# Performance work log

Hardware: AMD Instinct MI355X
Metric: run time of the kernel (lower is better)

## Reference

```python
import jax, jax.numpy as jnp
import numpy as np

PI = 3.141592653589793
DET_THRESHOLD = 0.25
MAX_DET = 100
REG_HEAD = 4
DEPTH_MEAN = 28.01  # smoke_coder.depth_ref[0]
DIM_REF = (3.88, 1.63, 1.53)  # smoke_coder.dim_ref[0] (l, h, w)


def setup_inputs() -> dict:
    key = jax.random.key(0)
    k1, k2, k3, k4 = jax.random.split(key, 4)
    B, C, H, W = 32, 3, 256, 832  # stride-4 feature map of 3328x1024 images
    pred_heatmap = jax.random.uniform(k1, (B, C, H, W), dtype=jnp.float32)
    pred_regression = jax.random.normal(k2, (B, C + 1, H, W), dtype=jnp.float32) * 0.1  # REG_HEAD=4 channels
    trans_mat = jnp.tile(jnp.array([[0.25, 0.0, 0.0], [0.0, 0.25, 0.0], [0.0, 0.0, 1.0]], jnp.float32), (B, 1, 1))
    K_mat = jnp.tile(jnp.array([[2100.0, 0.0, 1664.0], [0.0, 2100.0, 512.0], [0.0, 0.0, 1.0]], jnp.float32), (B, 1, 1))
    size = jnp.tile(jnp.array([3328.0, 1024.0], jnp.float32), (B, 1))  # (img_w, img_h)
    h_cam = jax.random.uniform(k3, (B,), jnp.float32, 1.4, 2.0)
    dimensions = jax.random.uniform(k4, (B, 3), jnp.float32, 1.5, 4.0)
    return dict(pred_heatmap=pred_heatmap, pred_regression=pred_regression, trans_mat=trans_mat,
                K_mat=K_mat, size=size, h_cam=h_cam, dimensions=dimensions)


def reference(pred_heatmap, pred_regression, trans_mat, K_mat, size, h_cam, dimensions):
    B, C, H, W = pred_heatmap.shape
    K = MAX_DET
    # ---- nms_hm: 3x3 max-pool, keep local maxima ----
    hmax = jax.lax.reduce_window(pred_heatmap, -jnp.inf, jax.lax.max, (1, 1, 3, 3), (1, 1, 1, 1), 'SAME')
    heat = pred_heatmap * (hmax == pred_heatmap).astype(pred_heatmap.dtype)
    # ---- select_topk: per-class topk then global topk ----
    scores_c, inds_c = jax.lax.top_k(heat.reshape(B, C, H * W), K)  # [B,C,K]
    ys_c = (inds_c // W).astype(jnp.float32)
    xs_c = (inds_c % W).astype(jnp.float32)
    scores, topk_ind = jax.lax.top_k(scores_c.reshape(B, C * K), K)  # [B,K]
    clses = (topk_ind // K).astype(jnp.float32)
    inds = jnp.take_along_axis(inds_c.reshape(B, C * K), topk_ind, axis=1)
    ys = jnp.take_along_axis(ys_c.reshape(B, C * K), topk_ind, axis=1)
    xs = jnp.take_along_axis(xs_c.reshape(B, C * K), topk_ind, axis=1)
    feat = pred_regression.reshape(B, REG_HEAD, H * W).transpose(0, 2, 1)  # [B,HW,R]
    pois = jnp.take_along_axis(feat, inds[:, :, None], axis=1).reshape(-1, REG_HEAD)  # [B*K,R]
    log_dv_delta = pois[:, 0]
    off_u = pois[:, 1]
    ori = pois[:, 2:]
    # ---- feature points -> image points via inverse affine ----
    pts = jnp.stack([xs.reshape(-1), ys.reshape(-1)], axis=1)
    pts = pts + jnp.stack([off_u, jnp.zeros_like(off_u)], axis=1)
    pts_h = jnp.concatenate([pts, jnp.ones((pts.shape[0], 1), pts.dtype)], axis=1)  # [N,3]
    obj = jnp.repeat(jnp.arange(B), K)
    trans_inv = jnp.linalg.inv(trans_mat)[obj]  # [N,3,3]
    img_pts = jnp.einsum('nij,nj->ni', trans_inv, pts_h)[:, :2]
    # ---- per-object camera params ----
    Ks = K_mat[obj]
    h = h_cam[obj]
    kd = dimensions[obj]
    fx, fy, cx = Ks[:, 0, 0], Ks[:, 1, 1], Ks[:, 0, 2]
    dim_ref = jnp.array(DIM_REF, jnp.float32)
    dims = jnp.where(jnp.isfinite(kd), kd, dim_ref[None, :])
    # ---- geometric depth decode ----
    h_ref = h - dims[:, 1] / 2.0
    log_dv_ref = jnp.log(jnp.clip(fy * jnp.abs(h_ref), 1e-7, None) / DEPTH_MEAN)
    log_dv = jnp.clip(log_dv_ref + log_dv_delta, -4.0, 8.0)
    depths = jnp.clip(fy * jnp.abs(h_ref) * jnp.exp(-log_dv), 0.5, 120.0)
    px = (img_pts[:, 0] - cx) * depths / fx
    locs = jnp.stack([px, h, depths], axis=1)  # [N,3]
    # ---- decode_orientation (SMOKE) ----
    rays = jnp.arctan(locs[:, 0] / (locs[:, 2] + 1e-7))
    alphas = jnp.arctan(ori[:, 0] / (ori[:, 1] + 1e-7))
    alphas = alphas + jnp.where(ori[:, 1] >= 0, -PI / 2, PI / 2)
    rotys = alphas + rays
    rotys = jnp.where(rotys > PI, rotys - 2 * PI, rotys)
    rotys = jnp.where(rotys < -PI, rotys + 2 * PI, rotys)
    # ---- encode_box2d: build 3D corners, rotate, project, clamp ----
    cos, sin = jnp.cos(rotys), jnp.sin(rotys)
    cx8 = jnp.array([-0.5, 0.5, 0.5, 0.5, 0.5, -0.5, -0.5, -0.5], jnp.float32)
    cy8 = jnp.array([-1.0, -1.0, 0.0, 0.0, -1.0, -1.0, 0.0, 0.0], jnp.float32)
    cz8 = jnp.array([-0.5, -0.5, -0.5, 0.5, 0.5, 0.5, 0.5, -0.5], jnp.float32)
    xc = dims[:, 0:1] * cx8  # l
    yc = dims[:, 1:2] * cy8  # h
    zc = dims[:, 2:3] * cz8  # w
    bx = cos[:, None] * xc + sin[:, None] * zc
    bz = -sin[:, None] * xc + cos[:, None] * zc
    box3d = jnp.stack([bx, yc, bz], axis=1) + locs[:, :, None]  # [N,3,8]
    proj = jnp.einsum('nij,njk->nik', Ks, box3d)
    uv = proj[:, :2, :] / proj[:, 2:3, :]
    img_w = size.reshape(-1)[0]
    img_h = size.reshape(-1)[1]
    xmins = jnp.clip(jnp.min(uv[:, 0, :], axis=1), 0.0, img_w)
    xmaxs = jnp.clip(jnp.max(uv[:, 0, :], axis=1), 0.0, img_w)
    ymins = jnp.clip(jnp.min(uv[:, 1, :], axis=1), 0.0, img_h)
    ymaxs = jnp.clip(jnp.max(uv[:, 1, :], axis=1), 0.0, img_h)
    box2d = jnp.stack([xmins, ymins, xmaxs, ymaxs], axis=1)
    pred_dims = jnp.roll(dims, -1, axis=1)  # (l,h,w)->(h,w,l)
    result = jnp.concatenate([clses.reshape(-1, 1), alphas[:, None], box2d, pred_dims, locs,
                              rotys[:, None], scores.reshape(-1, 1)], axis=1)  # [N,14]
    # fixed-shape equivalent of boolean filtering: zero out rows below threshold
    keep = (result[:, -1] > DET_THRESHOLD).astype(result.dtype)
    return result * keep[:, None]
```

## Files before the change

kernel.cpp:

```cpp
#include <hip/hip_runtime.h>
#include <math.h>

#define B_ 32
#define C_ 3
#define H_ 256
#define W_ 832
#define HW_ (H_*W_)
#define K_ 100
#define RPB 16
#define PARTS (H_/RPB)
#define NLOAD (W_/4)
#define BLK 256
#define CAP 2048
#define NCAND (C_*PARTS*K_)

typedef unsigned long long ull;

template<int N>
__device__ inline void bitonic_sort_desc(ull* s) {
    for (int k = 2; k <= N; k <<= 1) {
        for (int j = k >> 1; j > 0; j >>= 1) {
            __syncthreads();
            for (int i = threadIdx.x; i < N; i += BLK) {
                int ixj = i ^ j;
                if (ixj > i) {
                    ull a = s[i], b = s[ixj];
                    bool up = ((i & k) == 0);
                    if (up ? (a < b) : (a > b)) { s[i] = b; s[ixj] = a; }
                }
            }
        }
    }
    __syncthreads();
}

__device__ ull radix_select(const ull* __restrict__ buf, int cnt, int k) {
    __shared__ unsigned hist[256];
    __shared__ unsigned wsum[4];
    __shared__ ull pref_s;
    __shared__ int k_s;
    const int tid = threadIdx.x;
    const int lane = tid & 63;
    const int wv = tid >> 6;
    if (cnt < k) return 0ULL;
    if (tid == 0) { pref_s = 0ULL; k_s = k; }

    for (int pos = 7; pos >= 0; --pos) {
        __syncthreads();
        hist[tid] = 0;
        __syncthreads();
        const ull prefix = pref_s;
        const int kk = k_s;
        for (int i0 = 0; i0 < cnt; i0 += BLK) {
            const int i = i0 + tid;
            ull key = (i < cnt) ? buf[i] : 0ULL;
            bool todo = (i < cnt) &&
                        ((pos == 7) || ((key >> (8 * (pos + 1))) == prefix));
            unsigned d = (unsigned)(key >> (8 * pos)) & 255u;
            #pragma unroll
            for (int it = 0; it < 4; ++it) {
                const ull act = __ballot(todo);
                if (act == 0ULL) break;
                const int leader = __ffsll((long long)act) - 1;
                const unsigned dl = (unsigned)__shfl((int)d, leader);
                const bool same = todo && (d == dl);
                const ull ms = __ballot(same);
                if (lane == leader) atomicAdd(&hist[dl], (unsigned)__popcll(ms));
                if (same) todo = false;
            }
            if (todo) atomicAdd(&hist[d], 1u);
        }
        __syncthreads();
        const unsigned h = hist[tid];
        unsigned v = h;
        #pragma unroll
        for (int off = 1; off < 64; off <<= 1) {
            const unsigned o = __shfl_down(v, off);
            if (lane + off < 64) v += o;
        }
        if (lane == 0) wsum[wv] = v;
        __syncthreads();
        unsigned carry = 0;
        #pragma unroll
        for (int w = 0; w < 4; ++w) if (w > wv) carry += wsum[w];
        const unsigned S = v + carry;
        const unsigned above = S - h;
        if (S >= (unsigned)kk && above < (unsigned)kk) {
            pref_s = (prefix << 8) | (ull)tid;
            k_s = kk - (int)above;
        }
    }
    __syncthreads();
    return pref_s;
}

__global__ void __launch_bounds__(BLK) topk_part_kernel(
        const float* __restrict__ heat, ull* __restrict__ part_out) {
    const int chan = blockIdx.x / PARTS;
    const int c    = chan % C_;
    const int part = blockIdx.x % PARTS;
    const float* __restrict__ hp = heat + (size_t)chan * HW_;
    const int r0 = part * RPB;
    const int tid = threadIdx.x;
    const bool active = tid < NLOAD;
    const int x4 = tid * 4;
    const int lane = tid & 63;

    __shared__ float vmA[W_], vmB[W_];
    __shared__ ull buf[CAP];
    __shared__ int cnt;
    if (tid == 0) cnt = 0;

    float4 rA, rB, rC, rD;
    if (active) {
        const int ym1 = (r0 == 0) ? 0 : r0 - 1;
        rA = reinterpret_cast<const float4*>(hp + (size_t)ym1 * W_)[tid];
        rB = reinterpret_cast<const float4*>(hp + (size_t)r0  * W_)[tid];
        const int yp1 = (r0 == H_ - 1) ? r0 : r0 + 1;
        rC = reinterpret_cast<const float4*>(hp + (size_t)yp1 * W_)[tid];
    }
    __syncthreads();

    for (int r = 0; r < RPB; ++r) {
        const int y = r0 + r;
        float* vr = (r & 1) ? vmB : vmA;
        float4 vm;
        if (active) {
            const int yn = (y + 2 > H_ - 1) ? H_ - 1 : y + 2;
            rD = reinterpret_cast<const float4*>(hp + (size_t)yn * W_)[tid];
            vm.x = fmaxf(fmaxf(rA.x, rB.x), rC.x);
            vm.y = fmaxf(fmaxf(rA.y, rB.y), rC.y);
            vm.z = fmaxf(fmaxf(rA.z, rB.z), rC.z);
            vm.w = fmaxf(fmaxf(rA.w, rB.w), rC.w);
            reinterpret_cast<float4*>(&vr[x4])[0] = vm;
        }
        __syncthreads();
        {
            float left = -INFINITY, right = -INFINITY;
            float vv0 = 0.f, vv1 = 0.f, vv2 = 0.f, vv3 = 0.f;
            if (active) {
                left  = (tid == 0)         ? -INFINITY : vr[x4 - 1];
                right = (tid == NLOAD - 1) ? -INFINITY : vr[x4 + 4];
                vv0 = rB.x; vv1 = rB.y; vv2 = rB.z; vv3 = rB.w;
            }
            const float vn[6] = {left, vm.x, vm.y, vm.z, vm.w, right};
            const float vv[4] = {vv0, vv1, vv2, vv3};
            #pragma unroll
            for (int i = 0; i < 4; ++i) {
                const float v = vv[i];
                const bool peak = active && (v >= vn[i]) && (v >= vn[i+1]) && (v >= vn[i+2]);
                const ull m = __ballot(peak);
                if (peak) {
                    const unsigned p = (unsigned)(y * W_ + x4 + i);
                    const unsigned tie = ((unsigned)c << 18) | p;
                    const ull key = ((ull)__float_as_uint(v) << 32) | (ull)(~tie);
                    const int rank = __popcll(m & ((1ULL << lane) - 1ULL));
                    const int leader = __ffsll((long long)m) - 1;
                    int base = 0;
                    if (lane == leader) base = atomicAdd(&cnt, (int)__popcll(m));
                    base = __shfl(base, leader);
                    const int pos = base + rank;
                    if (pos < CAP) buf[pos] = key;
                }
            }
        }
        rA = rB; rB = rC; rC = rD;
    }
    __syncthreads();

    const int cc = (cnt < CAP) ? cnt : CAP;
    const ull thr = radix_select(buf, cc, K_);

    __shared__ int ocnt;
    if (tid == 0) ocnt = 0;
    __syncthreads();
    ull* o = part_out + (size_t)blockIdx.x * K_;
    for (int i0 = 0; i0 < cc; i0 += BLK) {
        const int i = i0 + tid;
        const ull key = (i < cc) ? buf[i] : 0ULL;
        const bool sel = (i < cc) && (key >= thr) && (key != 0ULL);
        const ull m = __ballot(sel);
        const int nsel = (int)__popcll(m);
        int base = 0;
        if (lane == 0 && nsel) base = atomicAdd(&ocnt, nsel);
        base = __shfl(base, 0);
        const int rank = (int)__popcll(m & ((1ULL << lane) - 1ULL));
        if (sel && base + rank < K_) o[base + rank] = key;
    }
    __syncthreads();
    const int oc = (ocnt < K_) ? ocnt : K_;
    for (int i = oc + tid; i < K_; i += BLK) o[i] = 0ULL;
}

__global__ void __launch_bounds__(BLK) merge_geom_kernel(
        const ull* __restrict__ part_keys, const float* __restrict__ reg,
        const float* __restrict__ trans, const float* __restrict__ Km,
        const float* __restrict__ sz, const float* __restrict__ hcam,
        const float* __restrict__ dimen, float* __restrict__ out) {
    const int b = blockIdx.x;
    const int tid = threadIdx.x;
    const int lane = tid & 63;
    __shared__ ull buf[NCAND];
    __shared__ ull sel_s[128];
    __shared__ int ocnt;
    const ull* src = part_keys + (size_t)b * NCAND;
    for (int i = tid; i < NCAND; i += BLK) buf[i] = src[i];
    if (tid < 128) sel_s[tid] = 0ULL;
    if (tid == 0) ocnt = 0;
    __syncthreads();

    const ull thr = radix_select(buf, NCAND, K_);
    for (int i0 = 0; i0 < NCAND; i0 += BLK) {
        const int i = i0 + tid;
        const ull key = (i < NCAND) ? buf[i] : 0ULL;
        const bool sel = (i < NCAND) && (key >= thr) && (key != 0ULL);
        const ull m = __ballot(sel);
        const int nsel = (int)__popcll(m);
        int base = 0;
        if (lane == 0 && nsel) base = atomicAdd(&ocnt, nsel);
        base = __shfl(base, 0);
        const int rank = (int)__popcll(m & ((1ULL << lane) - 1ULL));
        if (sel && base + rank < 128) sel_s[base + rank] = key;
    }
    bitonic_sort_desc<128>(sel_s);

    if (tid >= K_) return;
    const int n = b * K_ + tid;
    const ull key = sel_s[tid];
    const unsigned tie = ~(unsigned)(key & 0xFFFFFFFFULL);
    const float score = __uint_as_float((unsigned)(key >> 32));
    const float clsf  = (float)((tie >> 18) & 3u);
    unsigned hw = tie & 0x3FFFFu;
    if (hw >= HW_) hw = 0;
    const float xs = (float)(hw % W_);
    const float ys = (float)(hw / W_);

    const float* rg = reg + (size_t)b * 4 * HW_;
    const float delta = rg[hw];
    const float off_u = rg[HW_ + hw];
    const float ori0  = rg[2 * HW_ + hw];
    const float ori1  = rg[3 * HW_ + hw];

    const float* T = trans + b * 9;
    const float t00=T[0], t01=T[1], t02=T[2], t10=T[3], t11=T[4], t12=T[5],
                t20=T[6], t21=T[7], t22=T[8];
    const float det3 = t00*(t11*t22 - t12*t21) - t01*(t10*t22 - t12*t20)
                     + t02*(t10*t21 - t11*t20);
    const float idt = 1.0f / det3;
    const float i00 = (t11*t22 - t12*t21)*idt;
    const float i01 = (t02*t21 - t01*t22)*idt;
    const float i02 = (t01*t12 - t02*t11)*idt;

    const float pu = xs + off_u;
    const float img_x = i00*pu + i01*ys + i02;

    const float* Kb = Km + b * 9;
    const float k00=Kb[0],k01=Kb[1],k02=Kb[2],k10=Kb[3],k11=Kb[4],k12=Kb[5],
                k20=Kb[6],k21=Kb[7],k22=Kb[8];
    const float fx = k00, fy = k11, cx = k02;
    const float h = hcam[b];
    float d0 = dimen[b*3+0], d1 = dimen[b*3+1], d2 = dimen[b*3+2];
    if (!isfinite(d0)) d0 = 3.88f;
    if (!isfinite(d1)) d1 = 1.63f;
    if (!isfinite(d2)) d2 = 1.53f;

    const float h_ref = h - d1 * 0.5f;
    const float fyh = fy * fabsf(h_ref);
    const float log_dv_ref = logf(fmaxf(fyh, 1e-7f) / 28.01f);
    const float log_dv = fminf(fmaxf(log_dv_ref + delta, -4.0f), 8.0f);
    const float depth = fminf(fmaxf(fyh * expf(-log_dv), 0.5f), 120.0f);
    const float px = (img_x - cx) * depth / fx;

    const float PI_F = 3.14159265358979323846f;
    const float ray = atanf(px / (depth + 1e-7f));
    float alpha = atanf(ori0 / (ori1 + 1e-7f));
    alpha += (ori1 >= 0.0f) ? -1.5707963267948966f : 1.5707963267948966f;
    float roty = alpha + ray;
    if (roty >  PI_F) roty -= 6.283185307179586f;
    if (roty < -PI_F) roty += 6.283185307179586f;

    const float cosr = cosf(roty), sinr = sinf(roty);
    const float cx8[8] = {-0.5f, 0.5f, 0.5f, 0.5f, 0.5f,-0.5f,-0.5f,-0.5f};
    const float cy8[8] = {-1.0f,-1.0f, 0.0f, 0.0f,-1.0f,-1.0f, 0.0f, 0.0f};
    const float cz8[8] = {-0.5f,-0.5f,-0.5f, 0.5f, 0.5f, 0.5f, 0.5f,-0.5f};
    float umin = 1e30f, umax = -1e30f, vmin = 1e30f, vmax = -1e30f;
    #pragma unroll
    for (int i = 0; i < 8; ++i) {
        const float xc = d0 * cx8[i];
        const float yc = d1 * cy8[i];
        const float zc = d2 * cz8[i];
        const float X = cosr*xc + sinr*zc + px;
        const float Y = yc + h;
        const float Z = -sinr*xc + cosr*zc + depth;
        const float w = k20*X + k21*Y + k22*Z;
        const float u = (k00*X + k01*Y + k02*Z) / w;
        const float v = (k10*X + k11*Y + k12*Z) / w;
        umin = fminf(umin, u); umax = fmaxf(umax, u);
        vmin = fminf(vmin, v); vmax = fmaxf(vmax, v);
    }
    const float img_w = sz[0], img_h = sz[1];
    const float xmin = fminf(fmaxf(umin, 0.0f), img_w);
    const float xmax = fminf(fmaxf(umax, 0.0f), img_w);
    const float ymin = fminf(fmaxf(vmin, 0.0f), img_h);
    const float ymax = fminf(fmaxf(vmax, 0.0f), img_h);

    const float keep = (score > 0.25f) ? 1.0f : 0.0f;
    float* o = out + (size_t)n * 14;
    o[0]  = clsf  * keep;
    o[1]  = alpha * keep;
    o[2]  = xmin  * keep;
    o[3]  = ymin  * keep;
    o[4]  = xmax  * keep;
    o[5]  = ymax  * keep;
    o[6]  = d1    * keep;
    o[7]  = d2    * keep;
    o[8]  = d0    * keep;
    o[9]  = px    * keep;
    o[10] = h     * keep;
    o[11] = depth * keep;
    o[12] = roty  * keep;
    o[13] = score * keep;
}

extern "C" void kernel_launch(void* const* d_in, const int* in_sizes, int n_in,
                              void* d_out, int out_size, void* d_ws, size_t ws_size,
                              hipStream_t stream) {
    const float* heat  = (const float*)d_in[0];
    const float* reg   = (const float*)d_in[1];
    const float* trans = (const float*)d_in[2];
    const float* Kmat  = (const float*)d_in[3];
    const float* sz    = (const float*)d_in[4];
    const float* hcam  = (const float*)d_in[5];
    const float* dimen = (const float*)d_in[6];
    float* out = (float*)d_out;

    ull* part_keys = (ull*)d_ws;

    topk_part_kernel<<<B_ * C_ * PARTS, BLK, 0, stream>>>(heat, part_keys);
    merge_geom_kernel<<<B_, BLK, 0, stream>>>(
        part_keys, reg, trans, Kmat, sz, hcam, dimen, out);
}
```

Measured before the change: 268.1 us.

## Use wavefront shuffles for 3x3 NMS halo and compact radix-select candidates

Replaces the shared-memory vertical-max rows and their per-row block barrier with cross-lane shuffles. Wave-edge lanes load their halo columns directly from global memory. The radix select now compacts, after the upper 32 bits are fixed, the candidates that match the prefix into a small shared group, so the lower-byte passes scan fewer keys. This removes 16 block-wide syncs per block and shrinks the later histogram passes, at the cost of some extra scalar global loads and one extra compaction pass.

New measurement: 267.5 us. No clear change (-0.2%).

```diff
diff --git a/kernel.cpp b/kernel.cpp
--- a/kernel.cpp
+++ b/kernel.cpp
@@ -12,9 +12,14 @@
 #define NLOAD (W_/4)
 #define BLK 256
 #define CAP 2048
+#define GRP 256
 #define NCAND (C_*PARTS*K_)
 
 typedef unsigned long long ull;
+
+__device__ inline float fmax3(float a, float b, float c) {
+    return fmaxf(fmaxf(a, b), c);
+}
 
 template<int N>
 __device__ inline void bitonic_sort_desc(ull* s) {
@@ -39,22 +44,44 @@
     __shared__ unsigned wsum[4];
     __shared__ ull pref_s;
     __shared__ int k_s;
+    __shared__ ull grp[GRP];
+    __shared__ int gcnt;
     const int tid = threadIdx.x;
     const int lane = tid & 63;
     const int wv = tid >> 6;
     if (cnt < k) return 0ULL;
-    if (tid == 0) { pref_s = 0ULL; k_s = k; }
+    if (tid == 0) { pref_s = 0ULL; k_s = k; gcnt = 0; }
 
     for (int pos = 7; pos >= 0; --pos) {
         __syncthreads();
+        if (pos == 3) {
+            const ull hi = pref_s;
+            for (int i0 = 0; i0 < cnt; i0 += BLK) {
+                const int i = i0 + tid;
+                const ull key = (i < cnt) ? buf[i] : 0ULL;
+                const bool sel = (i < cnt) && ((key >> 32) == hi);
+                const ull m = __ballot(sel);
+                const int nsel = (int)__popcll(m);
+                int base = 0;
+                if (lane == 0 && nsel) base = atomicAdd(&gcnt, nsel);
+                base = __shfl(base, 0);
+                const int rank = (int)__popcll(m & ((1ULL << lane) - 1ULL));
+                if (sel && base + rank < GRP) grp[base + rank] = key;
+            }
+            __syncthreads();
+        }
+        const bool use_grp = (pos <= 3) && (gcnt <= GRP);
+        const ull* src = use_grp ? grp : buf;
+        const int scnt = use_grp ? gcnt : cnt;
+
         hist[tid] = 0;
         __syncthreads();
         const ull prefix = pref_s;
         const int kk = k_s;
-        for (int i0 = 0; i0 < cnt; i0 += BLK) {
+        for (int i0 = 0; i0 < scnt; i0 += BLK) {
             const int i = i0 + tid;
-            ull key = (i < cnt) ? buf[i] : 0ULL;
-            bool todo = (i < cnt) &&
+            ull key = (i < scnt) ? src[i] : 0ULL;
+            bool todo = (i < scnt) &&
                         ((pos == 7) || ((key >> (8 * (pos + 1))) == prefix));
             unsigned d = (unsigned)(key >> (8 * pos)) & 255u;
             #pragma unroll
@@ -106,49 +133,55 @@
     const int x4 = tid * 4;
     const int lane = tid & 63;
 
-    __shared__ float vmA[W_], vmB[W_];
     __shared__ ull buf[CAP];
     __shared__ int cnt;
     if (tid == 0) cnt = 0;
+    __syncthreads();
+
+    const bool needL = active && (lane == 0) && (tid != 0);
+    const bool needR = active && (lane == 63);
+    const int colL = x4 - 1;
+    const int colR = x4 + 4;
 
     float4 rA, rB, rC, rD;
-    if (active) {
+    float lA=0.f,lB=0.f,lC=0.f,lD=0.f, qA=0.f,qB=0.f,qC=0.f,qD=0.f;
+    {
         const int ym1 = (r0 == 0) ? 0 : r0 - 1;
-        rA = reinterpret_cast<const float4*>(hp + (size_t)ym1 * W_)[tid];
-        rB = reinterpret_cast<const float4*>(hp + (size_t)r0  * W_)[tid];
         const int yp1 = (r0 == H_ - 1) ? r0 : r0 + 1;
-        rC = reinterpret_cast<const float4*>(hp + (size_t)yp1 * W_)[tid];
-    }
-    __syncthreads();
+        if (active) {
+            rA = reinterpret_cast<const float4*>(hp + (size_t)ym1 * W_)[tid];
+            rB = reinterpret_cast<const float4*>(hp + (size_t)r0  * W_)[tid];
+            rC = reinterpret_cast<const float4*>(hp + (size_t)yp1 * W_)[tid];
+        }
+        if (needL) { lA = hp[ym1*W_+colL]; lB = hp[r0*W_+colL]; lC = hp[yp1*W_+colL]; }
+        if (needR) { qA = hp[ym1*W_+colR]; qB = hp[r0*W_+colR]; qC = hp[yp1*W_+colR]; }
+    }
 
     for (int r = 0; r < RPB; ++r) {
         const int y = r0 + r;
-        float* vr = (r & 1) ? vmB : vmA;
-        float4 vm;
+        const int yn = (y + 2 > H_ - 1) ? H_ - 1 : y + 2;
+        if (active) rD = reinterpret_cast<const float4*>(hp + (size_t)yn * W_)[tid];
+        if (needL) lD = hp[yn*W_+colL];
+        if (needR) qD = hp[yn*W_+colR];
+
         if (active) {
-            const int yn = (y + 2 > H_ - 1) ? H_ - 1 : y + 2;
-            rD = reinterpret_cast<const float4*>(hp + (size_t)yn * W_)[tid];
-            vm.x = fmaxf(fmaxf(rA.x, rB.x), rC.x);
-            vm.y = fmaxf(fmaxf(rA.y, rB.y), rC.y);
-            vm.z = fmaxf(fmaxf(rA.z, rB.z), rC.z);
-            vm.w = fmaxf(fmaxf(rA.w, rB.w), rC.w);
-            reinterpret_cast<float4*>(&vr[x4])[0] = vm;
-        }
-        __syncthreads();
-        {
-            float left = -INFINITY, right = -INFINITY;
-            float vv0 = 0.f, vv1 = 0.f, vv2 = 0.f, vv3 = 0.f;
-            if (active) {
-                left  = (tid == 0)         ? -INFINITY : vr[x4 - 1];
-                right = (tid == NLOAD - 1) ? -INFINITY : vr[x4 + 4];
-                vv0 = rB.x; vv1 = rB.y; vv2 = rB.z; vv3 = rB.w;
-            }
+            float4 vm;
+            vm.x = fmax3(rA.x, rB.x, rC.x);
+            vm.y = fmax3(rA.y, rB.y, rC.y);
+            vm.z = fmax3(rA.z, rB.z, rC.z);
+            vm.w = fmax3(rA.w, rB.w, rC.w);
+            float left  = __shfl_up(vm.w, 1);
+            float right = __shfl_down(vm.x, 1);
+            if (lane == 0)  left  = (tid == 0) ? -INFINITY : fmax3(lA, lB, lC);
+            if (lane == 63) right = fmax3(qA, qB, qC);
+            if (tid == NLOAD - 1) right = -INFINITY;
+
             const float vn[6] = {left, vm.x, vm.y, vm.z, vm.w, right};
-            const float vv[4] = {vv0, vv1, vv2, vv3};
+            const float vv[4] = {rB.x, rB.y, rB.z, rB.w};
             #pragma unroll
             for (int i = 0; i < 4; ++i) {
                 const float v = vv[i];
-                const bool peak = active && (v >= vn[i]) && (v >= vn[i+1]) && (v >= vn[i+2]);
+                const bool peak = (v >= vn[i]) && (v >= vn[i+1]) && (v >= vn[i+2]);
                 const ull m = __ballot(peak);
                 if (peak) {
                     const unsigned p = (unsigned)(y * W_ + x4 + i);
@@ -165,6 +198,8 @@
             }
         }
         rA = rB; rB = rC; rC = rD;
+        lA = lB; lB = lC; lC = lD;
+        qA = qB; qB = qC; qC = qD;
     }
     __syncthreads();
 
```
